# Performance work log

Measured on AMD Instinct MI355X. Metric: run time of the kernel, lower is better.

The kernel has to match this reference:

```python
import jax, jax.numpy as jnp
import numpy as np

N_NODES = 100000
N_EDGES = 1600000
D = 128
N_LAYERS = 3
N_GRAPHS = 128


def setup_inputs() -> dict:
    key = jax.random.key(0)
    ks = jax.random.split(key, 8)
    x = jax.random.normal(ks[0], (N_NODES, D), dtype=jnp.float32)
    # stacked GIN-MLP params (all layers are D->D since hidden_dim == in_dim)
    scale = 1.0 / np.sqrt(D)
    W1 = jax.random.normal(ks[1], (N_LAYERS, D, D), dtype=jnp.float32) * scale
    b1 = jax.random.normal(ks[2], (N_LAYERS, D), dtype=jnp.float32) * 0.01
    W2 = jax.random.normal(ks[3], (N_LAYERS, D, D), dtype=jnp.float32) * scale
    b2 = jax.random.normal(ks[4], (N_LAYERS, D), dtype=jnp.float32) * 0.01
    edge_index = jax.random.randint(ks[5], (2, N_EDGES), 0, N_NODES, dtype=jnp.int64)
    batch = jnp.sort(jax.random.randint(ks[6], (N_NODES,), 0, N_GRAPHS, dtype=jnp.int64))
    return {"x": x, "W1": W1, "b1": b1, "W2": W2, "b2": b2,
            "edge_index": edge_index, "batch": batch}


def reference(x, W1, b1, W2, b2, edge_index, batch):
    src = edge_index[0]
    dst = edge_index[1]
    n = x.shape[0]
    eps = jnp.float32(0.0)  # GIN eps (PyG default, not trained)
    for i in range(N_LAYERS):
        # gather neighbor features along edges, scatter-add to destination nodes
        agg = jax.ops.segment_sum(x[src], dst, num_segments=n)  # [N, D]
        h = (1.0 + eps) * x + agg
        h = jax.nn.relu(h @ W1[i] + b1[i])
        x = h @ W2[i] + b2[i]
    # sum-pool readout per graph
    h_G = jax.ops.segment_sum(x, batch, num_segments=N_GRAPHS)  # [G, D]
    return h_G
```

## Files before the change

### kernel.cpp

```cpp
#include <hip/hip_runtime.h>
#include <hip/hip_bf16.h>
#include <stdint.h>

#define N_NODES 100000
#define N_EDGES 1600000
#define DIM 128
#define N_GRAPHS 128
#define LDA 136

#define NBKT 392
#define BCAP 6144
#define BP   5632
#define IDXCAP 2048

#define NBIN_BLK 391
#define CVT_BLK 3125

typedef unsigned int uint32;
typedef unsigned short ushort16;

typedef __bf16 bf16x8 __attribute__((ext_vector_type(8)));
typedef float fx4 __attribute__((ext_vector_type(4)));

__device__ __forceinline__ float bfLo(uint32 u){ return __builtin_bit_cast(float, (uint32)(u << 16)); }
__device__ __forceinline__ float bfHi(uint32 u){ return __builtin_bit_cast(float, (uint32)(u & 0xFFFF0000u)); }
__device__ __forceinline__ ushort16 f2bf(float f){
  uint32 u = __builtin_bit_cast(uint32, f);
  u = u + 0x7FFFu + ((u >> 16) & 1u);
  return (ushort16)(u >> 16);
}
__device__ __forceinline__ uint32 pack2(float a, float b){
  return (uint32)f2bf(a) | ((uint32)f2bf(b) << 16);
}

__global__ __launch_bounds__(512) void k_prep(const float* __restrict__ x,
                                              const float* __restrict__ W1, const float* __restrict__ W2,
                                              const int* __restrict__ ei,
                                              ushort16* __restrict__ P, ushort16* __restrict__ Q,
                                              ushort16* __restrict__ Wf,
                                              int* __restrict__ bucketCursor,
                                              int* __restrict__ temp){
  __shared__ int hist[NBKT];
  __shared__ int base[NBKT];
  __shared__ int gbase[NBKT];
  __shared__ int scanbuf[512];
  __shared__ int sVal[4096];
  __shared__ unsigned short sBkt[4096];

  int bb = blockIdx.x;
  int t  = threadIdx.x;

  if (bb < NBIN_BLK){
    int e0 = bb * 4096;
    for (int i = t; i < NBKT; i += 512) hist[i] = 0;
    __syncthreads();

    int   myv[8];
    short myb[8];
    short myr[8];
    #pragma unroll
    for (int it = 0; it < 8; ++it){
      int e = e0 + it*512 + t;
      int v = 0; short b = -1; short r = 0;
      if (e < N_EDGES){
        int s = ei[e];
        int d = ei[N_EDGES + e];
        b = (short)(d >> 8);
        v = s | ((d & 255) << 17);
        r = (short)atomicAdd(&hist[b], 1);
      }
      myv[it] = v; myb[it] = b; myr[it] = r;
    }
    __syncthreads();

    scanbuf[t] = (t < NBKT) ? hist[t] : 0;
    __syncthreads();
    for (int off = 1; off < 512; off <<= 1){
      int x2 = 0;
      if (t >= off) x2 = scanbuf[t - off];
      __syncthreads();
      scanbuf[t] += x2;
      __syncthreads();
    }
    if (t < NBKT){
      base[t]  = scanbuf[t] - hist[t];
      gbase[t] = atomicAdd(&bucketCursor[t], hist[t]);
    }
    __syncthreads();

    #pragma unroll
    for (int it = 0; it < 8; ++it){
      if (myb[it] >= 0){
        int p = base[myb[it]] + myr[it];
        sVal[p] = myv[it];
        sBkt[p] = (unsigned short)myb[it];
      }
    }
    __syncthreads();

    int cnt = scanbuf[NBKT - 1];
    for (int p = t; p < cnt; p += 512){
      int b = sBkt[p];
      int g = gbase[b] + (p - base[b]);
      if (g < BCAP) temp[b*BCAP + g] = sVal[p];
    }
    return;
  }

  if (bb < NBIN_BLK + CVT_BLK){
    int idx = ((bb - NBIN_BLK)*512 + t) * 8;
    float4 v0 = *(const float4*)(x + idx);
    float4 v1 = *(const float4*)(x + idx + 4);
    uint4 o;
    o.x = pack2(v0.x, v0.y); o.y = pack2(v0.z, v0.w);
    o.z = pack2(v1.x, v1.y); o.w = pack2(v1.z, v1.w);
    *(uint4*)(P + idx) = o;
    return;
  }

  if (bb == NBIN_BLK + CVT_BLK){
    uint4 z = {0u,0u,0u,0u};
    if (t < 16)                *(uint4*)(P + (size_t)N_NODES*128 + t*8)      = z;
    else if (t < 32)           *(uint4*)(Q + (size_t)N_NODES*128 + (t-16)*8) = z;
    return;
  }

  int tid = (bb - (NBIN_BLK + CVT_BLK + 1))*512 + t;
  int layer = tid >> 12;
  int rem   = tid & 4095;
  int mat   = rem >> 11;
  int nt    = (rem >> 8) & 7;
  int kt    = (rem >> 6) & 3;
  int lane  = rem & 63;
  int kg = lane >> 4, m = lane & 15;
  int n  = nt*16 + m;
  int kb = kt*32 + kg*8;
  const float* src = (mat ? W2 : W1) + layer*16384;
  uint4 o;
  o.x = pack2(src[(kb+0)*128 + n], src[(kb+1)*128 + n]);
  o.y = pack2(src[(kb+2)*128 + n], src[(kb+3)*128 + n]);
  o.z = pack2(src[(kb+4)*128 + n], src[(kb+5)*128 + n]);
  o.w = pack2(src[(kb+6)*128 + n], src[(kb+7)*128 + n]);
  *(uint4*)(Wf + ((((size_t)(layer*2+mat)*8 + nt)*4 + kt)*64 + lane)*8) = o;
}

__global__ __launch_bounds__(512) void k_binB(const int* __restrict__ temp,
                                              const int* __restrict__ bucketCursor,
                                              int* __restrict__ rowptr,
                                              int* __restrict__ rowlen,
                                              int* __restrict__ colx){
  __shared__ int counts[256];
  __shared__ int sc[256];
  __shared__ int cur[256];
  __shared__ int stage[BCAP];
  __shared__ int sorted[BCAP];
  int b = blockIdx.x, t = threadIdx.x;
  int cnt = min(bucketCursor[b], BCAP);
  int gb  = b * BP;
  const int* src = temp + b*BCAP;

  if (t < 256) counts[t] = 0;
  __syncthreads();
  for (int p = t; p < cnt; p += 512){
    int v = src[p];
    stage[p] = v;
    atomicAdd(&counts[v >> 17], 1);
  }
  __syncthreads();

  int len = 0, plen = 0;
  if (t < 256){
    len  = counts[t];
    plen = (len + 3) & ~3;
    sc[t] = plen;
  }
  __syncthreads();
  for (int off = 1; off < 256; off <<= 1){
    int x = 0;
    if (t < 256 && t >= off) x = sc[t - off];
    __syncthreads();
    if (t < 256) sc[t] += x;
    __syncthreads();
  }
  int excl = 0;
  if (t < 256){
    excl = sc[t] - plen;
    cur[t] = excl;
    int node = b*256 + t;
    if (node < N_NODES){ rowptr[node] = gb + excl; rowlen[node] = plen; }
  }
  __syncthreads();

  for (int p = t; p < cnt; p += 512){
    int v = stage[p];
    int d = v >> 17;
    int pos = atomicAdd(&cur[d], 1);
    sorted[pos] = v & 0x1FFFF;
  }
  __syncthreads();

  if (t < 256){
    for (int k = len; k < plen; ++k) sorted[excl + k] = N_NODES;
  }
  __syncthreads();

  int total = min(sc[255], BP);
  for (int p = t; p < total; p += 512) colx[gb + p] = sorted[p];
}

__global__ __launch_bounds__(256, 6) void k_gin(const ushort16* __restrict__ xb, ushort16* __restrict__ hb,
                                                const ushort16* __restrict__ Wt1, const float* __restrict__ b1,
                                                const ushort16* __restrict__ Wt2, const float* __restrict__ b2,
                                                const int* __restrict__ rowptr, const int* __restrict__ rowlen,
                                                const int* __restrict__ colx){
  __shared__ __attribute__((aligned(16))) ushort16 sA[64 * LDA];
  __shared__ __attribute__((aligned(16))) int sIdx[IDXCAP];
  __shared__ int sOff[64];
  __shared__ int sLen[64];

  int t = threadIdx.x;
  int row0 = blockIdx.x * 64;
  int jBase = rowptr[row0];
  int lastV = min(row0 + 63, N_NODES - 1);
  int total = rowptr[lastV] + rowlen[lastV] - jBase;

  if (t < 64){
    int g = row0 + t;
    int off = 0, len = 0;
    if (g < N_NODES){ off = rowptr[g] - jBase; len = rowlen[g]; }
    sOff[t] = off; sLen[t] = len;
  }
  bool fast = (total <= IDXCAP);
  if (fast){
    for (int p = t; p < total; p += 256) sIdx[p] = colx[jBase + p];
  }
  __syncthreads();

  int wave = t >> 6, lane = t & 63;
  int g16 = lane >> 4, o = lane & 15;
  const uint32* xw = (const uint32*)xb;

#define GATH(r) (*(const uint4*)(xw + (size_t)(r)*64 + o*4))
#define ACC8(u) do { \
    a0 += (fx4){ bfLo((u).x), bfHi((u).x), bfLo((u).y), bfHi((u).y) }; \
    a1 += (fx4){ bfLo((u).z), bfHi((u).z), bfLo((u).w), bfHi((u).w) }; \
  } while(0)

  for (int q = 0; q < 4; ++q){
    int ln  = wave*16 + q*4 + g16;
    int off = sOff[ln];
    int len = sLen[ln];
    int gn  = row0 + ln;
    uint4 xv = {0u,0u,0u,0u};
    if (gn < N_NODES) xv = *(const uint4*)(xw + (size_t)gn*64 + o*4);
    fx4 a0 = (fx4){0.f,0.f,0.f,0.f};
    fx4 a1 = (fx4){0.f,0.f,0.f,0.f};

    if (fast){
      int rd = 0;
      for (; rd + 8 <= len; rd += 8){
        int i0 = sIdx[off+rd  ], i1 = sIdx[off+rd+1], i2 = sIdx[off+rd+2], i3 = sIdx[off+rd+3];
        int i4 = sIdx[off+rd+4], i5 = sIdx[off+rd+5], i6 = sIdx[off+rd+6], i7 = sIdx[off+rd+7];
        uint4 u0 = GATH(i0); uint4 u1 = GATH(i1); uint4 u2 = GATH(i2); uint4 u3 = GATH(i3);
        uint4 u4 = GATH(i4); uint4 u5 = GATH(i5); uint4 u6 = GATH(i6); uint4 u7 = GATH(i7);
        ACC8(u0); ACC8(u1); ACC8(u2); ACC8(u3);
        ACC8(u4); ACC8(u5); ACC8(u6); ACC8(u7);
      }
      if (rd < len){
        int i0 = sIdx[off+rd], i1 = sIdx[off+rd+1], i2 = sIdx[off+rd+2], i3 = sIdx[off+rd+3];
        uint4 u0 = GATH(i0); uint4 u1 = GATH(i1); uint4 u2 = GATH(i2); uint4 u3 = GATH(i3);
        ACC8(u0); ACC8(u1); ACC8(u2); ACC8(u3);
      }
    } else {
      for (int rd = 0; rd < len; rd += 4){
        int i0 = colx[jBase+off+rd], i1 = colx[jBase+off+rd+1];
        int i2 = colx[jBase+off+rd+2], i3 = colx[jBase+off+rd+3];
        uint4 u0 = GATH(i0); uint4 u1 = GATH(i1); uint4 u2 = GATH(i2); uint4 u3 = GATH(i3);
        ACC8(u0); ACC8(u1); ACC8(u2); ACC8(u3);
      }
    }

    uint4 r;
    r.x = pack2(a0[0]+bfLo(xv.x), a0[1]+bfHi(xv.x));
    r.y = pack2(a0[2]+bfLo(xv.y), a0[3]+bfHi(xv.y));
    r.z = pack2(a1[0]+bfLo(xv.z), a1[1]+bfHi(xv.z));
    r.w = pack2(a1[2]+bfLo(xv.w), a1[3]+bfHi(xv.w));
    *(uint4*)(sA + ln*LDA + o*8) = r;
  }
#undef GATH
#undef ACC8
  __syncthreads();

  int m = lane & 15, kg = lane >> 4;
  int n0 = wave * 2;

  bf16x8 bfa[4], bfb[4];
  #pragma unroll
  for (int kt = 0; kt < 4; ++kt){
    bfa[kt] = *(const bf16x8*)(Wt1 + (((n0+0)*4 + kt)*64 + lane)*8);
    bfb[kt] = *(const bf16x8*)(Wt1 + (((n0+1)*4 + kt)*64 + lane)*8);
  }

  fx4 acc[4][2];
  #pragma unroll
  for (int mt = 0; mt < 4; ++mt){ acc[mt][0] = (fx4){0,0,0,0}; acc[mt][1] = (fx4){0,0,0,0}; }

  #pragma unroll
  for (int kt = 0; kt < 4; ++kt){
    #pragma unroll
    for (int mt = 0; mt < 4; ++mt){
      bf16x8 av = *(const bf16x8*)(sA + (mt*16 + m)*LDA + kg*8 + kt*32);
      acc[mt][0] = __builtin_amdgcn_mfma_f32_16x16x32_bf16(av, bfa[kt], acc[mt][0], 0, 0, 0);
      acc[mt][1] = __builtin_amdgcn_mfma_f32_16x16x32_bf16(av, bfb[kt], acc[mt][1], 0, 0, 0);
    }
  }
  float bva = b1[(n0+0)*16 + m];
  float bvb = b1[(n0+1)*16 + m];
  __syncthreads();

  #pragma unroll
  for (int mt = 0; mt < 4; ++mt){
    #pragma unroll
    for (int r = 0; r < 4; ++r){
      int row = mt*16 + kg*4 + r;
      sA[row*LDA + (n0+0)*16 + m] = f2bf(fmaxf(acc[mt][0][r] + bva, 0.f));
      sA[row*LDA + (n0+1)*16 + m] = f2bf(fmaxf(acc[mt][1][r] + bvb, 0.f));
    }
  }
  #pragma unroll
  for (int kt = 0; kt < 4; ++kt){
    bfa[kt] = *(const bf16x8*)(Wt2 + (((n0+0)*4 + kt)*64 + lane)*8);
    bfb[kt] = *(const bf16x8*)(Wt2 + (((n0+1)*4 + kt)*64 + lane)*8);
  }
  float cva = b2[(n0+0)*16 + m];
  float cvb = b2[(n0+1)*16 + m];
  #pragma unroll
  for (int mt = 0; mt < 4; ++mt){ acc[mt][0] = (fx4){0,0,0,0}; acc[mt][1] = (fx4){0,0,0,0}; }
  __syncthreads();

  #pragma unroll
  for (int kt = 0; kt < 4; ++kt){
    #pragma unroll
    for (int mt = 0; mt < 4; ++mt){
      bf16x8 av = *(const bf16x8*)(sA + (mt*16 + m)*LDA + kg*8 + kt*32);
      acc[mt][0] = __builtin_amdgcn_mfma_f32_16x16x32_bf16(av, bfa[kt], acc[mt][0], 0, 0, 0);
      acc[mt][1] = __builtin_amdgcn_mfma_f32_16x16x32_bf16(av, bfb[kt], acc[mt][1], 0, 0, 0);
    }
  }

  #pragma unroll
  for (int mt = 0; mt < 4; ++mt){
    #pragma unroll
    for (int r = 0; r < 4; ++r){
      int row = row0 + mt*16 + kg*4 + r;
      if (row < N_NODES){
        hb[row*128 + (n0+0)*16 + m] = f2bf(acc[mt][0][r] + cva);
        hb[row*128 + (n0+1)*16 + m] = f2bf(acc[mt][1][r] + cvb);
      }
    }
  }
}

__device__ __forceinline__ int lower_bound_i(const int* __restrict__ a, int n, int key){
  int lo = 0, hi = n;
  while (lo < hi){ int mid = (lo + hi) >> 1; if (a[mid] < key) lo = mid + 1; else hi = mid; }
  return lo;
}

__global__ __launch_bounds__(256) void k_pool(const ushort16* __restrict__ xb, const int* __restrict__ batch,
                                              float* __restrict__ out){
  int g = blockIdx.x >> 2;
  int p = blockIdx.x & 3;
  int start = lower_bound_i(batch, N_NODES, g);
  int end   = lower_bound_i(batch, N_NODES, g + 1);
  int t = threadIdx.x;
  int c = t & 127;
  int h = t >> 7;
  float acc = 0.f;
  for (int r = start + p*2 + h; r < end; r += 8){
    uint32 u = (uint32)xb[r*128 + c];
    acc += __builtin_bit_cast(float, (uint32)(u << 16));
  }
  __shared__ float red[256];
  red[t] = acc; __syncthreads();
  if (t < 128) atomicAdd(&out[g*128 + c], red[t] + red[t + 128]);
}

extern "C" void kernel_launch(void* const* d_in, const int* in_sizes, int n_in,
                              void* d_out, int out_size, void* d_ws, size_t ws_size,
                              hipStream_t stream) {
  const float* x   = (const float*)d_in[0];
  const float* W1  = (const float*)d_in[1];
  const float* b1  = (const float*)d_in[2];
  const float* W2  = (const float*)d_in[3];
  const float* b2  = (const float*)d_in[4];
  const int*   ei  = (const int*)d_in[5];
  const int*   bat = (const int*)d_in[6];
  float* out = (float*)d_out;

  char* w = (char*)d_ws;
  auto carve = [&](size_t bytes) -> char* {
    char* p = w; w += (bytes + 255) & ~(size_t)255; return p;
  };
  ushort16* P    = (ushort16*)carve((size_t)(N_NODES+1) * DIM * 2);
  ushort16* Q    = (ushort16*)carve((size_t)(N_NODES+1) * DIM * 2);
  ushort16* Wf   = (ushort16*)carve((size_t)3 * 2 * 16384 * 2);
  int* rowptr    = (int*)carve((size_t)N_NODES * 4);
  int* rowlen    = (int*)carve((size_t)N_NODES * 4);
  int* colx      = (int*)carve((size_t)NBKT * BP * 4);
  int* bucketCursor = (int*)carve((NBKT + 1) * 4);
  int* temp      = (int*)Q;

  hipMemsetAsync(bucketCursor, 0, (NBKT + 1) * 4, stream);
  hipMemsetAsync(d_out, 0, (size_t)N_GRAPHS * DIM * 4, stream);

  k_prep<<<NBIN_BLK + CVT_BLK + 1 + 24, 512, 0, stream>>>(x, W1, W2, ei, P, Q, Wf,
                                                          bucketCursor, temp);
  k_binB<<<NBKT, 512, 0, stream>>>(temp, bucketCursor, rowptr, rowlen, colx);

  const int ginGrid = (N_NODES + 63) / 64;

  k_gin<<<ginGrid, 256, 0, stream>>>(P, Q, Wf + 0*16384, b1 + 0*128, Wf + 1*16384, b2 + 0*128,
                                     rowptr, rowlen, colx);
  k_gin<<<ginGrid, 256, 0, stream>>>(Q, P, Wf + 2*16384, b1 + 1*128, Wf + 3*16384, b2 + 1*128,
                                     rowptr, rowlen, colx);
  k_gin<<<ginGrid, 256, 0, stream>>>(P, Q, Wf + 4*16384, b1 + 2*128, Wf + 5*16384, b2 + 2*128,
                                     rowptr, rowlen, colx);

  k_pool<<<N_GRAPHS * 4, 256, 0, stream>>>(Q, bat, out);
}
```

Before: 358.9 us.

## Gather neighbors with a whole wave per node and drop LDS index staging

The aggregation loop now has a whole wave process one destination node at a time, with its four 16-lane groups each handling a different neighbor and then combining results with cross-lane shuffles. Before, each 16-lane group handled its own node. Column indices are read directly from global memory as int4 vectors instead of being staged in a shared-memory index buffer. Removing that buffer, and loading weights per k-step instead of holding them in registers, lowers LDS and register use, so launch bounds go from 6 to 8 blocks per SU. The risks are extra shuffle-reduction work per node, possible misaligned int4 reads, and less memory-level parallelism per lane.

Measured after the change: 362.9 us. Within noise of the previous version (+1.1%).

```diff
diff --git a/kernel.cpp b/kernel.cpp
--- a/kernel.cpp
+++ b/kernel.cpp
@@ -11,7 +11,6 @@
 #define NBKT 392
 #define BCAP 6144
 #define BP   5632
-#define IDXCAP 2048
 
 #define NBIN_BLK 391
 #define CVT_BLK 3125
@@ -208,110 +207,106 @@
   for (int p = t; p < total; p += 512) colx[gb + p] = sorted[p];
 }
 
-__global__ __launch_bounds__(256, 6) void k_gin(const ushort16* __restrict__ xb, ushort16* __restrict__ hb,
+__global__ __launch_bounds__(256, 8) void k_gin(const ushort16* __restrict__ xb, ushort16* __restrict__ hb,
                                                 const ushort16* __restrict__ Wt1, const float* __restrict__ b1,
                                                 const ushort16* __restrict__ Wt2, const float* __restrict__ b2,
                                                 const int* __restrict__ rowptr, const int* __restrict__ rowlen,
                                                 const int* __restrict__ colx){
   __shared__ __attribute__((aligned(16))) ushort16 sA[64 * LDA];
-  __shared__ __attribute__((aligned(16))) int sIdx[IDXCAP];
   __shared__ int sOff[64];
   __shared__ int sLen[64];
 
   int t = threadIdx.x;
   int row0 = blockIdx.x * 64;
-  int jBase = rowptr[row0];
-  int lastV = min(row0 + 63, N_NODES - 1);
-  int total = rowptr[lastV] + rowlen[lastV] - jBase;
 
   if (t < 64){
-    int g = row0 + t;
+    int gg = row0 + t;
     int off = 0, len = 0;
-    if (g < N_NODES){ off = rowptr[g] - jBase; len = rowlen[g]; }
+    if (gg < N_NODES){ off = rowptr[gg]; len = rowlen[gg]; }
     sOff[t] = off; sLen[t] = len;
   }
-  bool fast = (total <= IDXCAP);
-  if (fast){
-    for (int p = t; p < total; p += 256) sIdx[p] = colx[jBase + p];
-  }
   __syncthreads();
 
   int wave = t >> 6, lane = t & 63;
-  int g16 = lane >> 4, o = lane & 15;
+  int g = lane >> 4, o = lane & 15;
   const uint32* xw = (const uint32*)xb;
 
-#define GATH(r) (*(const uint4*)(xw + (size_t)(r)*64 + o*4))
-#define ACC8(u) do { \
-    a0 += (fx4){ bfLo((u).x), bfHi((u).x), bfLo((u).y), bfHi((u).y) }; \
-    a1 += (fx4){ bfLo((u).z), bfHi((u).z), bfLo((u).w), bfHi((u).w) }; \
-  } while(0)
-
-  for (int q = 0; q < 4; ++q){
-    int ln  = wave*16 + q*4 + g16;
-    int off = sOff[ln];
-    int len = sLen[ln];
-    int gn  = row0 + ln;
-    uint4 xv = {0u,0u,0u,0u};
-    if (gn < N_NODES) xv = *(const uint4*)(xw + (size_t)gn*64 + o*4);
-    fx4 a0 = (fx4){0.f,0.f,0.f,0.f};
-    fx4 a1 = (fx4){0.f,0.f,0.f,0.f};
-
-    if (fast){
-      int rd = 0;
-      for (; rd + 8 <= len; rd += 8){
-        int i0 = sIdx[off+rd  ], i1 = sIdx[off+rd+1], i2 = sIdx[off+rd+2], i3 = sIdx[off+rd+3];
-        int i4 = sIdx[off+rd+4], i5 = sIdx[off+rd+5], i6 = sIdx[off+rd+6], i7 = sIdx[off+rd+7];
-        uint4 u0 = GATH(i0); uint4 u1 = GATH(i1); uint4 u2 = GATH(i2); uint4 u3 = GATH(i3);
-        uint4 u4 = GATH(i4); uint4 u5 = GATH(i5); uint4 u6 = GATH(i6); uint4 u7 = GATH(i7);
-        ACC8(u0); ACC8(u1); ACC8(u2); ACC8(u3);
-        ACC8(u4); ACC8(u5); ACC8(u6); ACC8(u7);
+  for (int ni = 0; ni < 16; ++ni){
+    int ln  = wave*16 + ni;
+    int j   = __builtin_amdgcn_readfirstlane(sOff[ln]);
+    int end = j + __builtin_amdgcn_readfirstlane(sLen[ln]);
+
+    float f0=0.f,f1=0.f,f2=0.f,f3=0.f,f4=0.f,f5=0.f,f6=0.f,f7=0.f;
+
+    while (j + 8 <= end){
+      int4 c0 = *(const int4*)(colx + j);
+      int4 c1 = *(const int4*)(colx + j + 4);
+      int r0ab = (g & 1) ? c0.y : c0.x;
+      int r0cd = (g & 1) ? c0.w : c0.z;
+      int r0   = (g & 2) ? r0cd : r0ab;
+      int r1ab = (g & 1) ? c1.y : c1.x;
+      int r1cd = (g & 1) ? c1.w : c1.z;
+      int r1   = (g & 2) ? r1cd : r1ab;
+      uint4 u0 = *(const uint4*)(xw + (size_t)r0*64 + o*4);
+      uint4 u1 = *(const uint4*)(xw + (size_t)r1*64 + o*4);
+      f0 += bfLo(u0.x); f1 += bfHi(u0.x); f2 += bfLo(u0.y); f3 += bfHi(u0.y);
+      f4 += bfLo(u0.z); f5 += bfHi(u0.z); f6 += bfLo(u0.w); f7 += bfHi(u0.w);
+      f0 += bfLo(u1.x); f1 += bfHi(u1.x); f2 += bfLo(u1.y); f3 += bfHi(u1.y);
+      f4 += bfLo(u1.z); f5 += bfHi(u1.z); f6 += bfLo(u1.w); f7 += bfHi(u1.w);
+      j += 8;
+    }
+    if (j < end){
+      int4 c0 = *(const int4*)(colx + j);
+      int rab = (g & 1) ? c0.y : c0.x;
+      int rcd = (g & 1) ? c0.w : c0.z;
+      int r0  = (g & 2) ? rcd : rab;
+      uint4 u0 = *(const uint4*)(xw + (size_t)r0*64 + o*4);
+      f0 += bfLo(u0.x); f1 += bfHi(u0.x); f2 += bfLo(u0.y); f3 += bfHi(u0.y);
+      f4 += bfLo(u0.z); f5 += bfHi(u0.z); f6 += bfLo(u0.w); f7 += bfHi(u0.w);
+    }
+
+    f0 += __shfl_xor(f0, 16, 64); f1 += __shfl_xor(f1, 16, 64);
+    f2 += __shfl_xor(f2, 16, 64); f3 += __shfl_xor(f3, 16, 64);
+    f4 += __shfl_xor(f4, 16, 64); f5 += __shfl_xor(f5, 16, 64);
+    f6 += __shfl_xor(f6, 16, 64); f7 += __shfl_xor(f7, 16, 64);
+    f0 += __shfl_xor(f0, 32, 64); f1 += __shfl_xor(f1, 32, 64);
+    f2 += __shfl_xor(f2, 32, 64); f3 += __shfl_xor(f3, 32, 64);
+    f4 += __shfl_xor(f4, 32, 64); f5 += __shfl_xor(f5, 32, 64);
+    f6 += __shfl_xor(f6, 32, 64); f7 += __shfl_xor(f7, 32, 64);
+
+    if (g == 0){
+      int gn = row0 + ln;
+      uint4 r;
+      if (gn < N_NODES){
+        uint4 xv = *(const uint4*)(xw + (size_t)gn*64 + o*4);
+        r.x = pack2(f0 + bfLo(xv.x), f1 + bfHi(xv.x));
+        r.y = pack2(f2 + bfLo(xv.y), f3 + bfHi(xv.y));
+        r.z = pack2(f4 + bfLo(xv.z), f5 + bfHi(xv.z));
+        r.w = pack2(f6 + bfLo(xv.w), f7 + bfHi(xv.w));
+      } else {
+        r.x = r.y = r.z = r.w = 0u;
       }
-      if (rd < len){
-        int i0 = sIdx[off+rd], i1 = sIdx[off+rd+1], i2 = sIdx[off+rd+2], i3 = sIdx[off+rd+3];
-        uint4 u0 = GATH(i0); uint4 u1 = GATH(i1); uint4 u2 = GATH(i2); uint4 u3 = GATH(i3);
-        ACC8(u0); ACC8(u1); ACC8(u2); ACC8(u3);
-      }
-    } else {
-      for (int rd = 0; rd < len; rd += 4){
-        int i0 = colx[jBase+off+rd], i1 = colx[jBase+off+rd+1];
-        int i2 = colx[jBase+off+rd+2], i3 = colx[jBase+off+rd+3];
-        uint4 u0 = GATH(i0); uint4 u1 = GATH(i1); uint4 u2 = GATH(i2); uint4 u3 = GATH(i3);
-        ACC8(u0); ACC8(u1); ACC8(u2); ACC8(u3);
-      }
-    }
-
-    uint4 r;
-    r.x = pack2(a0[0]+bfLo(xv.x), a0[1]+bfHi(xv.x));
-    r.y = pack2(a0[2]+bfLo(xv.y), a0[3]+bfHi(xv.y));
-    r.z = pack2(a1[0]+bfLo(xv.z), a1[1]+bfHi(xv.z));
-    r.w = pack2(a1[2]+bfLo(xv.w), a1[3]+bfHi(xv.w));
-    *(uint4*)(sA + ln*LDA + o*8) = r;
-  }
-#undef GATH
-#undef ACC8
+      *(uint4*)(sA + ln*LDA + o*8) = r;
+    }
+  }
   __syncthreads();
 
   int m = lane & 15, kg = lane >> 4;
   int n0 = wave * 2;
 
-  bf16x8 bfa[4], bfb[4];
+  fx4 acc[4][2];
+  #pragma unroll
+  for (int mt = 0; mt < 4; ++mt){ acc[mt][0] = (fx4){0,0,0,0}; acc[mt][1] = (fx4){0,0,0,0}; }
+
   #pragma unroll
   for (int kt = 0; kt < 4; ++kt){
-    bfa[kt] = *(const bf16x8*)(Wt1 + (((n0+0)*4 + kt)*64 + lane)*8);
-    bfb[kt] = *(const bf16x8*)(Wt1 + (((n0+1)*4 + kt)*64 + lane)*8);
-  }
-
-  fx4 acc[4][2];
-  #pragma unroll
-  for (int mt = 0; mt < 4; ++mt){ acc[mt][0] = (fx4){0,0,0,0}; acc[mt][1] = (fx4){0,0,0,0}; }
-
-  #pragma unroll
-  for (int kt = 0; kt < 4; ++kt){
+    bf16x8 ba = *(const bf16x8*)(Wt1 + (((n0+0)*4 + kt)*64 + lane)*8);
+    bf16x8 bb = *(const bf16x8*)(Wt1 + (((n0+1)*4 + kt)*64 + lane)*8);
     #pragma unroll
     for (int mt = 0; mt < 4; ++mt){
       bf16x8 av = *(const bf16x8*)(sA + (mt*16 + m)*LDA + kg*8 + kt*32);
-      acc[mt][0] = __builtin_amdgcn_mfma_f32_16x16x32_bf16(av, bfa[kt], acc[mt][0], 0, 0, 0);
-      acc[mt][1] = __builtin_amdgcn_mfma_f32_16x16x32_bf16(av, bfb[kt], acc[mt][1], 0, 0, 0);
+      acc[mt][0] = __builtin_amdgcn_mfma_f32_16x16x32_bf16(av, ba, acc[mt][0], 0, 0, 0);
+      acc[mt][1] = __builtin_amdgcn_mfma_f32_16x16x32_bf16(av, bb, acc[mt][1], 0, 0, 0);
     }
   }
   float bva = b1[(n0+0)*16 + m];
@@ -327,11 +322,6 @@
       sA[row*LDA + (n0+1)*16 + m] = f2bf(fmaxf(acc[mt][1][r] + bvb, 0.f));
     }
   }
-  #pragma unroll
-  for (int kt = 0; kt < 4; ++kt){
-    bfa[kt] = *(const bf16x8*)(Wt2 + (((n0+0)*4 + kt)*64 + lane)*8);
-    bfb[kt] = *(const bf16x8*)(Wt2 + (((n0+1)*4 + kt)*64 + lane)*8);
-  }
   float cva = b2[(n0+0)*16 + m];
   float cvb = b2[(n0+1)*16 + m];
   #pragma unroll
@@ -340,11 +330,13 @@
 
   #pragma unroll
   for (int kt = 0; kt < 4; ++kt){
+    bf16x8 ba = *(const bf16x8*)(Wt2 + (((n0+0)*4 + kt)*64 + lane)*8);
+    bf16x8 bb = *(const bf16x8*)(Wt2 + (((n0+1)*4 + kt)*64 + lane)*8);
     #pragma unroll
     for (int mt = 0; mt < 4; ++mt){
       bf16x8 av = *(const bf16x8*)(sA + (mt*16 + m)*LDA + kg*8 + kt*32);
-      acc[mt][0] = __builtin_amdgcn_mfma_f32_16x16x32_bf16(av, bfa[kt], acc[mt][0], 0, 0, 0);
-      acc[mt][1] = __builtin_amdgcn_mfma_f32_16x16x32_bf16(av, bfb[kt], acc[mt][1], 0, 0, 0);
+      acc[mt][0] = __builtin_amdgcn_mfma_f32_16x16x32_bf16(av, ba, acc[mt][0], 0, 0, 0);
+      acc[mt][1] = __builtin_amdgcn_mfma_f32_16x16x32_bf16(av, bb, acc[mt][1], 0, 0, 0);
     }
   }
 
```
